# Performance work log

Hardware: AMD Instinct MI355X
Metric: run time of the kernel (lower is better)

Reference implementation:

```python
import jax, jax.numpy as jnp
import numpy as np

N = 50000      # nodes
E = 800000     # edges
D = 256        # hidden_dim (input node features)
A = 128        # attention_dim = attention_ratio * heads
H = 8          # heads
DK = A // H    # 16


def setup_inputs() -> dict:
    key = jax.random.key(0)
    ks = jax.random.split(key, 6)
    x = jax.random.normal(ks[0], (N, D), dtype=jnp.float32)
    # small weight scale keeps exp(pre) well-conditioned (module uses tiny const init)
    Wq = jax.random.normal(ks[1], (A, D), dtype=jnp.float32) * 0.02
    bq = jnp.full((A,), 0.01, dtype=jnp.float32)
    Wk = jax.random.normal(ks[2], (A, D), dtype=jnp.float32) * 0.02
    bk = jnp.full((A,), 0.01, dtype=jnp.float32)
    edge_index = jax.random.randint(ks[3], (2, E), 0, N, dtype=jnp.int32)
    # d0_index[1] holds the two node indices each duplicated edge score scatters to
    d0_index = jax.random.randint(ks[4], (2, 2 * E), 0, N, dtype=jnp.int32)
    return {"x": x, "Wq": Wq, "bq": bq, "Wk": Wk, "bk": bk,
            "edge_index": edge_index, "d0_index": d0_index}


def reference(x, Wq, bq, Wk, bk, edge_index, d0_index):
    # linear projections -> [N, H, DK]
    q = (x @ Wq.T + bq).reshape(N, H, DK)
    k = (x @ Wk.T + bk).reshape(N, H, DK)
    src, dst = edge_index[0], edge_index[1]
    q_i = q[src]   # [E, H, DK]
    k_j = k[dst]
    q_j = q[dst]
    k_i = k[src]
    # symmetrized scaled-dot attention score per edge/head
    pre = 0.5 * jnp.sum(q_i * k_j + q_j * k_i, axis=-1)  # [E, H]
    pre = jnp.mean(pre, axis=-1)                          # [E]
    diagA1 = jnp.exp(pre)
    # duplicate each edge score: (a, a, b, b, ...) == torch (view(-1,1)*ones(E,2)).view(-1)
    edge_score_per_node = jnp.repeat(diagA1, 2)           # [2E]
    diagA0 = jax.ops.segment_sum(edge_score_per_node, d0_index[1], num_segments=N)
    return diagA0, diagA1
```

## Files before the change

kernel.cpp:

```cpp
#include <hip/hip_runtime.h>
#include <hip/hip_bf16.h>

#define N_NODES 50000
#define N_EDGES 800000
#define DIM 256
#define QKDIM 256
#define NB_T  391
#define CAP   8192
#define ITEMS (2 * N_EDGES)
#define IPB   4096

typedef __bf16 bfrag  __attribute__((ext_vector_type(8)));
typedef __bf16 bf4    __attribute__((ext_vector_type(4)));
typedef float  ffrag  __attribute__((ext_vector_type(4)));
typedef float  f2     __attribute__((ext_vector_type(2)));
typedef float  f4v    __attribute__((ext_vector_type(4)));

#define EP_PITCH 272

__global__ __launch_bounds__(256) void prep_bin(
    const float* __restrict__ Wq, const float* __restrict__ Wk,
    __bf16* __restrict__ Wb,
    const int* __restrict__ d0, unsigned int* __restrict__ rec,
    int* __restrict__ cur)
{
    __shared__ int lcnt[NB_T];
    __shared__ int lbase[NB_T];
    const int tid = threadIdx.x;
    const int gtid = blockIdx.x * 256 + tid;

    const int i4 = gtid * 4;
    if (i4 < 65536) {
        const float* s = (i4 < 32768) ? (Wq + i4) : (Wk + (i4 - 32768));
        const float4 v = *(const float4*)s;
        bf4 o;
        o[0] = (__bf16)v.x; o[1] = (__bf16)v.y; o[2] = (__bf16)v.z; o[3] = (__bf16)v.w;
        *(bf4*)(Wb + i4) = o;
    }

    for (int b = tid; b < NB_T; b += 256) lcnt[b] = 0;
    __syncthreads();
    const int base = blockIdx.x * IPB;
    int tg[16];
    #pragma unroll
    for (int r = 0; r < 16; ++r) {
        const int i = base + r * 256 + tid;
        tg[r] = (i < ITEMS) ? d0[i] : -1;
        if (tg[r] >= 0) atomicAdd(&lcnt[tg[r] >> 7], 1);
    }
    __syncthreads();

    for (int b = tid; b < NB_T; b += 256) {
        const int c = lcnt[b];
        lbase[b] = c ? atomicAdd(&cur[b], c) : 0;
    }
    __syncthreads();
    for (int b = tid; b < NB_T; b += 256) lcnt[b] = 0;
    __syncthreads();

    #pragma unroll
    for (int r = 0; r < 16; ++r) {
        if (tg[r] >= 0) {
            const int i = base + r * 256 + tid;
            const int b = tg[r] >> 7;
            const int off = atomicAdd(&lcnt[b], 1);
            rec[(size_t)b * CAP + lbase[b] + off] =
                ((unsigned int)(tg[r] & 127) << 20) | (unsigned int)(i >> 1);
        }
    }
}

__global__ __launch_bounds__(256) void proj_mfma(
    const float* __restrict__ x,
    const __bf16* __restrict__ Wb,
    const float* __restrict__ bq, const float* __restrict__ bk,
    unsigned char* __restrict__ qk8)
{
    __shared__ __bf16 As[64 * 256];

    const int tid  = threadIdx.x;
    const int wv   = tid >> 6;
    const int lane = tid & 63;
    const int m    = lane & 15;
    const int q    = lane >> 4;
    const int mbase = blockIdx.x * 64;

    {
        const int srow = tid >> 2;
        const int c4   = tid & 3;
        int grow = mbase + srow;
        grow = grow < N_NODES ? grow : N_NODES - 1;
        const float* xp = x + (size_t)grow * DIM;
        const int mt_ = srow >> 4, m_ = srow & 15;
        #pragma unroll
        for (int i = 0; i < 16; ++i) {
            const int k = c4 * 4 + 16 * i;
            const f4v v = __builtin_nontemporal_load((const f4v*)(xp + k));
            bf4 o;
            o[0] = (__bf16)v[0]; o[1] = (__bf16)v[1];
            o[2] = (__bf16)v[2]; o[3] = (__bf16)v[3];
            const int seg = (k >> 5) * 4 + mt_;
            const int ln  = ((k >> 3) & 3) * 16 + m_;
            *(bf4*)(As + seg * 512 + ln * 8 + (k & 7)) = o;
        }
    }
    __syncthreads();

    ffrag acc[4][4] = {};

    #pragma unroll
    for (int h = 0; h < 2; ++h) {
        bfrag b[4][4];
        #pragma unroll
        for (int sp = 0; sp < 4; ++sp)
            #pragma unroll
            for (int nt = 0; nt < 4; ++nt) {
                const int col = wv * 64 + nt * 16 + m;
                b[sp][nt] = *(const bfrag*)(Wb + (size_t)col * DIM
                                            + 32 * (4 * h + sp) + 8 * q);
            }
        #pragma unroll
        for (int sp = 0; sp < 4; ++sp) {
            bfrag a[4];
            #pragma unroll
            for (int mt = 0; mt < 4; ++mt)
                a[mt] = *(const bfrag*)(As + ((4 * h + sp) * 4 + mt) * 512 + lane * 8);
            #pragma unroll
            for (int mt = 0; mt < 4; ++mt)
                #pragma unroll
                for (int nt = 0; nt < 4; ++nt)
                    acc[mt][nt] = __builtin_amdgcn_mfma_f32_16x16x32_bf16(
                                      a[mt], b[sp][nt], acc[mt][nt], 0, 0, 0);
        }
    }

    __syncthreads();
    unsigned char* ep = (unsigned char*)As;
    #pragma unroll
    for (int nt = 0; nt < 4; ++nt) {
        const int col  = wv * 64 + nt * 16 + m;
        const float bias = (col < 128) ? bq[col] : bk[col - 128];
        #pragma unroll
        for (int mt = 0; mt < 4; ++mt) {
            #pragma unroll
            for (int r = 0; r < 4; ++r) {
                const int rl = mt * 16 + q * 4 + r;
                const float v = acc[mt][nt][r] + bias;
                const int pk = __builtin_amdgcn_cvt_pk_fp8_f32(v, v, 0, false);
                ep[rl * EP_PITCH + col] = (unsigned char)(pk & 0xFF);
            }
        }
    }
    __syncthreads();
    {
        const int rl = tid >> 2;
        const int ch = tid & 3;
        const int grow = mbase + rl;
        if (grow < N_NODES) {
            const uint4* s4 = (const uint4*)(ep + rl * EP_PITCH + ch * 64);
            const uint4 t0 = s4[0], t1 = s4[1], t2 = s4[2], t3 = s4[3];
            uint4* g = (uint4*)(qk8 + (size_t)grow * QKDIM + ch * 64);
            g[0] = t0; g[1] = t1; g[2] = t2; g[3] = t3;
        }
    }
}

__global__ __launch_bounds__(256) void edge_compute(
    const unsigned char* __restrict__ qk8,
    const int* __restrict__ edge_index,
    float* __restrict__ out)
{
    const int wave = (blockIdx.x * blockDim.x + threadIdx.x) >> 6;
    const int lane = threadIdx.x & 63;
    const int g = lane >> 2;
    const int j = lane & 3;
    const int e = wave * 16 + g;

    const int src = __builtin_nontemporal_load(edge_index + e);
    const int dst = __builtin_nontemporal_load(edge_index + N_EDGES + e);

    const uint4* rs = (const uint4*)(qk8 + (size_t)src * QKDIM);
    const uint4* rd = (const uint4*)(qk8 + (size_t)dst * QKDIM);

    uint4 a[4], b[4];
    #pragma unroll
    for (int i = 0; i < 4; ++i) a[i] = rs[4 * i + j];
    #pragma unroll
    for (int i = 0; i < 4; ++i) b[i] = rd[4 * ((i + 2) & 3) + j];

    f2 acc = {0.f, 0.f};
    #pragma unroll
    for (int i = 0; i < 4; ++i) {
        const unsigned int* ua = (const unsigned int*)&a[i];
        const unsigned int* ub = (const unsigned int*)&b[i];
        #pragma unroll
        for (int t = 0; t < 4; ++t) {
            const f2 x0 = __builtin_amdgcn_cvt_pk_f32_fp8(ua[t], false);
            const f2 y0 = __builtin_amdgcn_cvt_pk_f32_fp8(ub[t], false);
            const f2 x1 = __builtin_amdgcn_cvt_pk_f32_fp8(ua[t], true);
            const f2 y1 = __builtin_amdgcn_cvt_pk_f32_fp8(ub[t], true);
            acc += x0 * y0;
            acc += x1 * y1;
        }
    }
    float p = acc[0] + acc[1];

    p += __shfl_xor(p, 1, 64);
    p += __shfl_xor(p, 2, 64);

    if (j == 0)
        out[N_NODES + e] = __expf(p * 0.0625f);
}

__global__ __launch_bounds__(1024) void phase_scatter(
    const unsigned int* __restrict__ rec, const int* __restrict__ cur,
    float* __restrict__ out)
{
    __shared__ float acc[128];
    const int b = blockIdx.x;
    const int tid = threadIdx.x;
    if (tid < 128) acc[tid] = 0.f;
    __syncthreads();

    const int cnt = cur[b];
    const unsigned int* rb = rec + (size_t)b * CAP;
    for (int i = tid; i < cnt; i += 1024) {
        const unsigned int r = rb[i];
        const float v = out[N_NODES + (r & 0xFFFFF)];
        atomicAdd(&acc[r >> 20], v);
    }
    __syncthreads();

    if (tid < 128) {
        const int n = b * 128 + tid;
        if (n < N_NODES) out[n] = acc[tid];
    }
}

extern "C" void kernel_launch(void* const* d_in, const int* in_sizes, int n_in,
                              void* d_out, int out_size, void* d_ws, size_t ws_size,
                              hipStream_t stream) {
    const float* x  = (const float*)d_in[0];
    const float* Wq = (const float*)d_in[1];
    const float* bq = (const float*)d_in[2];
    const float* Wk = (const float*)d_in[3];
    const float* bk = (const float*)d_in[4];
    const int* edge_index = (const int*)d_in[5];
    const int* d0 = (const int*)d_in[6] + 2 * N_EDGES;
    float* out = (float*)d_out;

    char* w = (char*)d_ws;
    unsigned char* qk8 = (unsigned char*)w;  w += (size_t)N_NODES * QKDIM;
    __bf16* Wb = (__bf16*)w;                 w += 131072;
    unsigned int* rec = (unsigned int*)w;    w += (size_t)NB_T * CAP * 4;
    int* cur = (int*)w;                      w += 2048;

    hipMemsetAsync(cur, 0, NB_T * sizeof(int), stream);
    prep_bin<<<NB_T, 256, 0, stream>>>(Wq, Wk, Wb, d0, rec, cur);
    proj_mfma<<<(N_NODES + 63) / 64, 256, 0, stream>>>(x, Wb, bq, bk, qk8);
    edge_compute<<<N_EDGES / 64, 256, 0, stream>>>(qk8, edge_index, out);
    phase_scatter<<<NB_T, 1024, 0, stream>>>(rec, cur, out);
}
```

Measured before the change: 205.9 us.

## Merge projection and binning into one launch, per-wave LDS scatter accumulators

Merges the weight-conversion, binning and projection kernels into one launch. Projection blocks convert fp32 weights to bf16 on the fly, and the remaining blocks do the d0 binning concurrently, which removes a kernel launch and the dependency between the two. The scatter kernel now keeps 16 per-wave LDS accumulators that are reduced at the end, to cut shared-atomic contention. A fallback path using global atomics is added for small workspaces. The cost is redundant weight conversion in every projection block.

```diff
diff --git a/kernel.cpp b/kernel.cpp
--- a/kernel.cpp
+++ b/kernel.cpp
@@ -9,6 +9,7 @@
 #define CAP   8192
 #define ITEMS (2 * N_EDGES)
 #define IPB   4096
+#define PROJ_BLOCKS 782
 
 typedef __bf16 bfrag  __attribute__((ext_vector_type(8)));
 typedef __bf16 bf4    __attribute__((ext_vector_type(4)));
@@ -18,29 +19,124 @@
 
 #define EP_PITCH 272
 
-__global__ __launch_bounds__(256) void prep_bin(
+__global__ __launch_bounds__(256) void prep_proj(
+    const float* __restrict__ x,
     const float* __restrict__ Wq, const float* __restrict__ Wk,
-    __bf16* __restrict__ Wb,
+    const float* __restrict__ bq, const float* __restrict__ bk,
+    unsigned char* __restrict__ qk8,
     const int* __restrict__ d0, unsigned int* __restrict__ rec,
-    int* __restrict__ cur)
+    int* __restrict__ cur, int do_bin)
 {
-    __shared__ int lcnt[NB_T];
-    __shared__ int lbase[NB_T];
+    __shared__ unsigned char smem[32768];
     const int tid = threadIdx.x;
-    const int gtid = blockIdx.x * 256 + tid;
-
-    const int i4 = gtid * 4;
-    if (i4 < 65536) {
-        const float* s = (i4 < 32768) ? (Wq + i4) : (Wk + (i4 - 32768));
-        const float4 v = *(const float4*)s;
-        bf4 o;
-        o[0] = (__bf16)v.x; o[1] = (__bf16)v.y; o[2] = (__bf16)v.z; o[3] = (__bf16)v.w;
-        *(bf4*)(Wb + i4) = o;
-    }
+
+    if (blockIdx.x < PROJ_BLOCKS) {
+        __bf16* As = (__bf16*)smem;
+        const int wv   = tid >> 6;
+        const int lane = tid & 63;
+        const int m    = lane & 15;
+        const int q    = lane >> 4;
+        const int mbase = blockIdx.x * 64;
+
+        {
+            const int srow = tid >> 2;
+            const int c4   = tid & 3;
+            int grow = mbase + srow;
+            grow = grow < N_NODES ? grow : N_NODES - 1;
+            const float* xp = x + (size_t)grow * DIM;
+            const int mt_ = srow >> 4, m_ = srow & 15;
+            #pragma unroll
+            for (int i = 0; i < 16; ++i) {
+                const int k = c4 * 4 + 16 * i;
+                const f4v v = __builtin_nontemporal_load((const f4v*)(xp + k));
+                bf4 o;
+                o[0] = (__bf16)v[0]; o[1] = (__bf16)v[1];
+                o[2] = (__bf16)v[2]; o[3] = (__bf16)v[3];
+                const int seg = (k >> 5) * 4 + mt_;
+                const int ln  = ((k >> 3) & 3) * 16 + m_;
+                *(bf4*)(As + seg * 512 + ln * 8 + (k & 7)) = o;
+            }
+        }
+        __syncthreads();
+
+        ffrag acc[4][4] = {};
+
+        #pragma unroll
+        for (int h = 0; h < 2; ++h) {
+            bfrag b[4][4];
+            #pragma unroll
+            for (int sp = 0; sp < 4; ++sp)
+                #pragma unroll
+                for (int nt = 0; nt < 4; ++nt) {
+                    const int col = wv * 64 + nt * 16 + m;
+                    const float* wrow = (col < 128)
+                        ? (Wq + (size_t)col * DIM)
+                        : (Wk + (size_t)(col - 128) * DIM);
+                    const int k0 = 32 * (4 * h + sp) + 8 * q;
+                    const float4 f0 = *(const float4*)(wrow + k0);
+                    const float4 f1 = *(const float4*)(wrow + k0 + 4);
+                    bfrag o;
+                    o[0] = (__bf16)f0.x; o[1] = (__bf16)f0.y;
+                    o[2] = (__bf16)f0.z; o[3] = (__bf16)f0.w;
+                    o[4] = (__bf16)f1.x; o[5] = (__bf16)f1.y;
+                    o[6] = (__bf16)f1.z; o[7] = (__bf16)f1.w;
+                    b[sp][nt] = o;
+                }
+            #pragma unroll
+            for (int sp = 0; sp < 4; ++sp) {
+                bfrag a[4];
+                #pragma unroll
+                for (int mt = 0; mt < 4; ++mt)
+                    a[mt] = *(const bfrag*)(As + ((4 * h + sp) * 4 + mt) * 512 + lane * 8);
+                #pragma unroll
+                for (int mt = 0; mt < 4; ++mt)
+                    #pragma unroll
+                    for (int nt = 0; nt < 4; ++nt)
+                        acc[mt][nt] = __builtin_amdgcn_mfma_f32_16x16x32_bf16(
+                                          a[mt], b[sp][nt], acc[mt][nt], 0, 0, 0);
+            }
+        }
+
+        __syncthreads();
+        unsigned char* ep = (unsigned char*)As;
+        #pragma unroll
+        for (int nt = 0; nt < 4; ++nt) {
+            const int col  = wv * 64 + nt * 16 + m;
+            const float bias = (col < 128) ? bq[col] : bk[col - 128];
+            #pragma unroll
+            for (int mt = 0; mt < 4; ++mt) {
+                #pragma unroll
+                for (int r = 0; r < 4; ++r) {
+                    const int rl = mt * 16 + q * 4 + r;
+                    const float v = acc[mt][nt][r] + bias;
+                    const int pk = __builtin_amdgcn_cvt_pk_fp8_f32(v, v, 0, false);
+                    ep[rl * EP_PITCH + col] = (unsigned char)(pk & 0xFF);
+                }
+            }
+        }
+        __syncthreads();
+        {
+            const int rl = tid >> 2;
+            const int ch = tid & 3;
+            const int grow = mbase + rl;
+            if (grow < N_NODES) {
+                const uint4* s4 = (const uint4*)(ep + rl * EP_PITCH + ch * 64);
+                const uint4 t0 = s4[0], t1 = s4[1], t2 = s4[2], t3 = s4[3];
+                uint4* g = (uint4*)(qk8 + (size_t)grow * QKDIM + ch * 64);
+                g[0] = t0; g[1] = t1; g[2] = t2; g[3] = t3;
+            }
+        }
+        return;
+    }
+
+    if (!do_bin) return;
+    int* lcnt  = (int*)smem;
+    int* lbase = (int*)(smem + 2048);
+    const int pb = blockIdx.x - PROJ_BLOCKS;
 
     for (int b = tid; b < NB_T; b += 256) lcnt[b] = 0;
     __syncthreads();
-    const int base = blockIdx.x * IPB;
+    const int base = pb * IPB;
     int tg[16];
     #pragma unroll
     for (int r = 0; r < 16; ++r) {
@@ -49,7 +145,6 @@
         if (tg[r] >= 0) atomicAdd(&lcnt[tg[r] >> 7], 1);
     }
     __syncthreads();
-
     for (int b = tid; b < NB_T; b += 256) {
         const int c = lcnt[b];
         lbase[b] = c ? atomicAdd(&cur[b], c) : 0;
@@ -57,7 +152,6 @@
     __syncthreads();
     for (int b = tid; b < NB_T; b += 256) lcnt[b] = 0;
     __syncthreads();
-
     #pragma unroll
     for (int r = 0; r < 16; ++r) {
         if (tg[r] >= 0) {
@@ -66,101 +160,6 @@
             const int off = atomicAdd(&lcnt[b], 1);
             rec[(size_t)b * CAP + lbase[b] + off] =
                 ((unsigned int)(tg[r] & 127) << 20) | (unsigned int)(i >> 1);
-        }
-    }
-}
-
-__global__ __launch_bounds__(256) void proj_mfma(
-    const float* __restrict__ x,
-    const __bf16* __restrict__ Wb,
-    const float* __restrict__ bq, const float* __restrict__ bk,
-    unsigned char* __restrict__ qk8)
-{
-    __shared__ __bf16 As[64 * 256];
-
-    const int tid  = threadIdx.x;
-    const int wv   = tid >> 6;
-    const int lane = tid & 63;
-    const int m    = lane & 15;
-    const int q    = lane >> 4;
-    const int mbase = blockIdx.x * 64;
-
-    {
-        const int srow = tid >> 2;
-        const int c4   = tid & 3;
-        int grow = mbase + srow;
-        grow = grow < N_NODES ? grow : N_NODES - 1;
-        const float* xp = x + (size_t)grow * DIM;
-        const int mt_ = srow >> 4, m_ = srow & 15;
-        #pragma unroll
-        for (int i = 0; i < 16; ++i) {
-            const int k = c4 * 4 + 16 * i;
-            const f4v v = __builtin_nontemporal_load((const f4v*)(xp + k));
-            bf4 o;
-            o[0] = (__bf16)v[0]; o[1] = (__bf16)v[1];
-            o[2] = (__bf16)v[2]; o[3] = (__bf16)v[3];
-            const int seg = (k >> 5) * 4 + mt_;
-            const int ln  = ((k >> 3) & 3) * 16 + m_;
-            *(bf4*)(As + seg * 512 + ln * 8 + (k & 7)) = o;
-        }
-    }
-    __syncthreads();
-
-    ffrag acc[4][4] = {};
-
-    #pragma unroll
-    for (int h = 0; h < 2; ++h) {
-        bfrag b[4][4];
-        #pragma unroll
-        for (int sp = 0; sp < 4; ++sp)
-            #pragma unroll
-            for (int nt = 0; nt < 4; ++nt) {
-                const int col = wv * 64 + nt * 16 + m;
-                b[sp][nt] = *(const bfrag*)(Wb + (size_t)col * DIM
-                                            + 32 * (4 * h + sp) + 8 * q);
-            }
-        #pragma unroll
-        for (int sp = 0; sp < 4; ++sp) {
-            bfrag a[4];
-            #pragma unroll
-            for (int mt = 0; mt < 4; ++mt)
-                a[mt] = *(const bfrag*)(As + ((4 * h + sp) * 4 + mt) * 512 + lane * 8);
-            #pragma unroll
-            for (int mt = 0; mt < 4; ++mt)
-                #pragma unroll
-                for (int nt = 0; nt < 4; ++nt)
-                    acc[mt][nt] = __builtin_amdgcn_mfma_f32_16x16x32_bf16(
-                                      a[mt], b[sp][nt], acc[mt][nt], 0, 0, 0);
-        }
-    }
-
-    __syncthreads();
-    unsigned char* ep = (unsigned char*)As;
-    #pragma unroll
-    for (int nt = 0; nt < 4; ++nt) {
-        const int col  = wv * 64 + nt * 16 + m;
-        const float bias = (col < 128) ? bq[col] : bk[col - 128];
-        #pragma unroll
-        for (int mt = 0; mt < 4; ++mt) {
-            #pragma unroll
-            for (int r = 0; r < 4; ++r) {
-                const int rl = mt * 16 + q * 4 + r;
-                const float v = acc[mt][nt][r] + bias;
-                const int pk = __builtin_amdgcn_cvt_pk_fp8_f32(v, v, 0, false);
-                ep[rl * EP_PITCH + col] = (unsigned char)(pk & 0xFF);
-            }
-        }
-    }
-    __syncthreads();
-    {
-        const int rl = tid >> 2;
-        const int ch = tid & 3;
-        const int grow = mbase + rl;
-        if (grow < N_NODES) {
-            const uint4* s4 = (const uint4*)(ep + rl * EP_PITCH + ch * 64);
-            const uint4 t0 = s4[0], t1 = s4[1], t2 = s4[2], t3 = s4[3];
-            uint4* g = (uint4*)(qk8 + (size_t)grow * QKDIM + ch * 64);
-            g[0] = t0; g[1] = t1; g[2] = t2; g[3] = t3;
         }
     }
 }
@@ -204,22 +203,70 @@
         }
     }
     float p = acc[0] + acc[1];
-
     p += __shfl_xor(p, 1, 64);
     p += __shfl_xor(p, 2, 64);
 
     if (j == 0)
         out[N_NODES + e] = __expf(p * 0.0625f);
+}
+
+__global__ __launch_bounds__(256) void edge_atomic(
+    const unsigned char* __restrict__ qk8,
+    const int* __restrict__ edge_index, const int* __restrict__ d0,
+    float* __restrict__ out)
+{
+    const int wave = (blockIdx.x * blockDim.x + threadIdx.x) >> 6;
+    const int lane = threadIdx.x & 63;
+    const int g = lane >> 2, j = lane & 3;
+    const int e = wave * 16 + g;
+
+    const int src = edge_index[e];
+    const int dst = edge_index[N_EDGES + e];
+
+    const uint4* rs = (const uint4*)(qk8 + (size_t)src * QKDIM);
+    const uint4* rd = (const uint4*)(qk8 + (size_t)dst * QKDIM);
+
+    uint4 a[4], b[4];
+    #pragma unroll
+    for (int i = 0; i < 4; ++i) a[i] = rs[4 * i + j];
+    #pragma unroll
+    for (int i = 0; i < 4; ++i) b[i] = rd[4 * ((i + 2) & 3) + j];
+
+    f2 acc = {0.f, 0.f};
+    #pragma unroll
+    for (int i = 0; i < 4; ++i) {
+        const unsigned int* ua = (const unsigned int*)&a[i];
+        const unsigned int* ub = (const unsigned int*)&b[i];
+        #pragma unroll
+        for (int t = 0; t < 4; ++t) {
+            const f2 x0 = __builtin_amdgcn_cvt_pk_f32_fp8(ua[t], false);
+            const f2 y0 = __builtin_amdgcn_cvt_pk_f32_fp8(ub[t], false);
+            const f2 x1 = __builtin_amdgcn_cvt_pk_f32_fp8(ua[t], true);
+            const f2 y1 = __builtin_amdgcn_cvt_pk_f32_fp8(ub[t], true);
+            acc += x0 * y0;
+            acc += x1 * y1;
+        }
+    }
+    float p = acc[0] + acc[1];
+    p += __shfl_xor(p, 1, 64);
+    p += __shfl_xor(p, 2, 64);
+
+    if (j < 2) {
+        const float val = __expf(p * 0.0625f);
+        if (j == 0) out[N_NODES + e] = val;
+        atomicAdd(&out[d0[2 * e + j]], val);
+    }
 }
 
 __global__ __launch_bounds__(1024) void phase_scatter(
     const unsigned int* __restrict__ rec, const int* __restrict__ cur,
     float* __restrict__ out)
 {
-    __shared__ float acc[128];
+    __shared__ float acc[16][128];
     const int b = blockIdx.x;
     const int tid = threadIdx.x;
-    if (tid < 128) acc[tid] = 0.f;
+    const int wid = tid >> 6;
+    for (int i = tid; i < 16 * 128; i += 1024) ((float*)acc)[i] = 0.f;
     __syncthreads();
 
     const int cnt = cur[b];
@@ -227,13 +274,16 @@
     for (int i = tid; i < cnt; i += 1024) {
         const unsigned int r = rb[i];
         const float v = out[N_NODES + (r & 0xFFFFF)];
-        atomicAdd(&acc[r >> 20], v);
+        atomicAdd(&acc[wid][r >> 20], v);
     }
     __syncthreads();
 
     if (tid < 128) {
+        float s = 0.f;
+        #pragma unroll
+        for (int w = 0; w < 16; ++w) s += acc[w][tid];
         const int n = b * 128 + tid;
-        if (n < N_NODES) out[n] = acc[tid];
+        if (n < N_NODES) out[n] = s;
     }
 }
 
@@ -251,13 +301,22 @@
 
     char* w = (char*)d_ws;
     unsigned char* qk8 = (unsigned char*)w;  w += (size_t)N_NODES * QKDIM;
-    __bf16* Wb = (__bf16*)w;                 w += 131072;
     unsigned int* rec = (unsigned int*)w;    w += (size_t)NB_T * CAP * 4;
     int* cur = (int*)w;                      w += 2048;
 
-    hipMemsetAsync(cur, 0, NB_T * sizeof(int), stream);
-    prep_bin<<<NB_T, 256, 0, stream>>>(Wq, Wk, Wb, d0, rec, cur);
-    proj_mfma<<<(N_NODES + 63) / 64, 256, 0, stream>>>(x, Wb, bq, bk, qk8);
-    edge_compute<<<N_EDGES / 64, 256, 0, stream>>>(qk8, edge_index, out);
-    phase_scatter<<<NB_T, 1024, 0, stream>>>(rec, cur, out);
-}
+    const size_t need = (size_t)(w - (char*)d_ws);
+    const int use_bin = (ws_size >= need) ? 1 : 0;
+
+    if (use_bin) {
+        hipMemsetAsync(cur, 0, NB_T * sizeof(int), stream);
+        prep_proj<<<PROJ_BLOCKS + NB_T, 256, 0, stream>>>(
+            x, Wq, Wk, bq, bk, qk8, d0, rec, cur, 1);
+        edge_compute<<<N_EDGES / 64, 256, 0, stream>>>(qk8, edge_index, out);
+        phase_scatter<<<NB_T, 1024, 0, stream>>>(rec, cur, out);
+    } else {
+        hipMemsetAsync(out, 0, N_NODES * sizeof(float), stream);
+        prep_proj<<<PROJ_BLOCKS, 256, 0, stream>>>(
+            x, Wq, Wk, bq, bk, qk8, d0, (unsigned int*)qk8, (int*)qk8, 0);
+        edge_atomic<<<N_EDGES / 64, 256, 0, stream>>>(qk8, edge_index, d0, out);
+    }
+}
```

Measured after the change: 205.8 us. About the same (-0.0%).
